# Kernel tuning notes

Hardware: AMD Instinct MI355X
Metric: run time of the kernel (lower is better)

Reference implementation:

```python
import jax, jax.numpy as jnp
import numpy as np
from functools import partial

TAU = 2.0          # LIFNode default tau
V_TH = 1.0         # default v_threshold
ALPHA = 2.0        # SoftSign surrogate default alpha (unused in fwd; heaviside forward)

T, B, F = 256, 64, 1024


@jax.custom_vjp
def soft_sign_spike(x):
    # forward: heaviside; backward: SoftSign surrogate gradient
    return (x >= 0).astype(x.dtype)

def _sss_fwd(x):
    return (x >= 0).astype(x.dtype), x

def _sss_bwd(x, g):
    grad = g * (ALPHA / 2.0) / jnp.square(1.0 + jnp.abs(ALPHA * x))
    return (grad,)

soft_sign_spike.defvjp(_sss_fwd, _sss_bwd)


def setup_inputs() -> dict:
    key = jax.random.key(0)
    k1, k2 = jax.random.split(key)
    # binary input spikes, as an SNN would receive
    input_spikes = (jax.random.uniform(k1, (T, B, F)) < 0.5).astype(jnp.float32)
    # torch.nn.Linear weight [out_features, in_features], Kaiming-uniform-ish init
    bound = 1.0 / np.sqrt(F)
    W = jax.random.uniform(k2, (F, F), minval=-bound, maxval=bound, dtype=jnp.float32)
    return {"input_spikes": input_spikes, "W": W}


def reference(input_spikes, W):
    # batch the per-timestep Linear into one GEMM: y = x @ W.T
    cur = jnp.einsum("tbf,gf->tbg", input_spikes, W)  # [T, B, F]

    def step(v, x):
        # decay_input=True, v_reset=0: v = v + (x - v) / tau
        v = v + (x - v) / TAU
        s = soft_sign_spike(v - V_TH)
        # hard reset to v_reset=0 (detach_reset=False)
        v = (1.0 - s) * v
        return v, s

    v0 = jnp.zeros(cur.shape[1:], dtype=cur.dtype)
    _, out = jax.lax.scan(step, v0, cur)
    return out  # [T, B, F] output spikes
```

## Files before the change

kernel.cpp:

```cpp
#include <hip/hip_runtime.h>
#include <stdint.h>


#define T_STEPS 256
#define M_DIM 16384
#define N_DIM 1024
#define K_DIM 1024
#define PLANE 65536

typedef int v4i  __attribute__((ext_vector_type(4)));
typedef int v16i __attribute__((ext_vector_type(16)));
typedef unsigned int u32;
typedef unsigned long long u64;

#define AB_BYTES   (M_DIM * K_DIM)
#define AB_LIMB    AB_BYTES
#define WS_AB      (AB_BYTES + 4 * (1 << 20))
#define MT_BITS    (M_DIM * 128)
#define WS_MT      (MT_BITS + 4 * (1 << 20))

__device__ __forceinline__ void gload_lds16(const void* g, void* l) {
    __builtin_amdgcn_global_load_lds(
        (const __attribute__((address_space(1))) u32*)g,
        (__attribute__((address_space(3))) u32*)l, 16, 0, 0);
}

__global__ __launch_bounds__(256) void prep_bytes_f(const float* __restrict__ X,
                                                    uint4* __restrict__ af) {
    const int gid  = blockIdx.x * 256 + threadIdx.x;
    const int lane = gid & 63;
    const int fs   = gid >> 6;
    const int m    = (fs >> 5) * 32 + (lane & 31);
    const int k    = (fs & 31) * 32 + (lane >> 5) * 16;
    const float4* src = reinterpret_cast<const float4*>(X + (size_t)m * K_DIM + k);
    uint4 r;
    u32* pr = &r.x;
    #pragma unroll
    for (int q = 0; q < 4; ++q) {
        const float4 f = src[q];
        pr[q] = (f.x != 0.f ? 1u : 0u) | (f.y != 0.f ? 0x100u : 0u) |
                (f.z != 0.f ? 0x10000u : 0u) | (f.w != 0.f ? 0x1000000u : 0u);
    }
    af[gid] = r;
}

__global__ __launch_bounds__(256) void prep_limbs_f(const float* __restrict__ W,
                                                    char* __restrict__ bf) {
    const int gid  = blockIdx.x * 256 + threadIdx.x;
    const int lane = gid & 63;
    const int fs   = gid >> 6;
    const int n    = (fs >> 5) * 32 + (lane & 31);
    const int k    = (fs & 31) * 32 + (lane >> 5) * 16;
    const float* src = W + (size_t)n * K_DIM + k;
    u32 w0[4] = {}, w1[4] = {}, w2[4] = {}, w3[4] = {};
    #pragma unroll
    for (int e = 0; e < 16; ++e) {
        const double d = (double)src[e] * 34359738368.0;
        long long kq = llrint(d);
        const int8_t l0 = (int8_t)kq; kq = (kq - l0) >> 8;
        const int8_t l1 = (int8_t)kq; kq = (kq - l1) >> 8;
        const int8_t l2 = (int8_t)kq; kq = (kq - l2) >> 8;
        const int8_t l3 = (int8_t)kq;
        const int sh = (e & 3) * 8, wd = e >> 2;
        w0[wd] |= ((u32)(uint8_t)l0) << sh;
        w1[wd] |= ((u32)(uint8_t)l1) << sh;
        w2[wd] |= ((u32)(uint8_t)l2) << sh;
        w3[wd] |= ((u32)(uint8_t)l3) << sh;
    }
    char* base = bf + (size_t)fs * 4096 + lane * 16;
    *(uint4*)(base)        = make_uint4(w0[0], w0[1], w0[2], w0[3]);
    *(uint4*)(base + 1024) = make_uint4(w1[0], w1[1], w1[2], w1[3]);
    *(uint4*)(base + 2048) = make_uint4(w2[0], w2[1], w2[2], w2[3]);
    *(uint4*)(base + 3072) = make_uint4(w3[0], w3[1], w3[2], w3[3]);
}

__global__ __launch_bounds__(256, 2) void gemm_i8_f(
    const char* __restrict__ af, const char* __restrict__ bf,
    float* __restrict__ out) {
    __shared__ __align__(16) char lds[2][16384];

    const int tid  = threadIdx.x;
    const int lane = tid & 63;
    const int w    = tid >> 6;
    const int l31  = lane & 31;
    const int lh   = lane >> 5;

    const int L   = blockIdx.x;
    const int xcd = L & 7;
    const int j   = L >> 3;
    const int bm  = xcd * 8 + (j & 7);
    const int bn  = j >> 3;

    v16i acc[2][4] = {};

    const char* gB = bf + ((size_t)(bn * 32 + w) * 4) * 1024 + lane * 16;
    const int   lB = (w * 4) * 1024 + lane * 16;

    const char* gA0 = af + ((size_t)(bm * 8 + 2 * w) * 32) * 1024 + lane * 16;
    const char* gA1 = gA0 + 32 * 1024;

    v4i aw0[4], aw1[4], an0[4], an1[4];

    #pragma unroll
    for (int lb = 0; lb < 4; ++lb)
        gload_lds16(gB + lb * 1024, (char*)lds[0] + lB + lb * 1024);
    #pragma unroll
    for (int ks = 0; ks < 4; ++ks) {
        aw0[ks] = *(const v4i*)(gA0 + ks * 1024);
        aw1[ks] = *(const v4i*)(gA1 + ks * 1024);
    }
    __syncthreads();

    #pragma unroll
    for (int c = 0; c < 8; ++c) {
        const char* rb = lds[c & 1];
        char* wb = (char*)lds[(c & 1) ^ 1];
        if (c < 7) {
            #pragma unroll
            for (int lb = 0; lb < 4; ++lb)
                gload_lds16(gB + (size_t)(c + 1) * 16384 + lb * 1024,
                            wb + lB + lb * 1024);
            #pragma unroll
            for (int ks = 0; ks < 4; ++ks) {
                an0[ks] = *(const v4i*)(gA0 + (c + 1) * 4096 + ks * 1024);
                an1[ks] = *(const v4i*)(gA1 + (c + 1) * 4096 + ks * 1024);
            }
        }
        #pragma unroll
        for (int ks = 0; ks < 4; ++ks) {
            #pragma unroll
            for (int lb = 0; lb < 4; ++lb) {
                const v4i b = *(const v4i*)(rb + (ks * 4 + lb) * 1024 + lane * 16);
                acc[0][lb] = __builtin_amdgcn_mfma_i32_32x32x32_i8(aw0[ks], b, acc[0][lb], 0, 0, 0);
                acc[1][lb] = __builtin_amdgcn_mfma_i32_32x32x32_i8(aw1[ks], b, acc[1][lb], 0, 0, 0);
            }
        }
        __syncthreads();
        if (c < 7) {
            #pragma unroll
            for (int ks = 0; ks < 4; ++ks) { aw0[ks] = an0[ks]; aw1[ks] = an1[ks]; }
        }
    }

    const int n = bn * 32 + l31;
    #pragma unroll
    for (int i = 0; i < 2; ++i) {
        #pragma unroll
        for (int r = 0; r < 16; ++r) {
            const double s = (double)acc[i][0][r] + 256.0 * (double)acc[i][1][r] +
                             65536.0 * (double)acc[i][2][r] +
                             16777216.0 * (double)acc[i][3][r];
            const float cur = (float)(s * 2.9103830456733704e-11);
            const int row = (r & 3) + 8 * (r >> 2) + 4 * lh;
            const int m = bm * 256 + (2 * w + i) * 32 + row;
            out[(size_t)m * N_DIM + n] = cur;
        }
    }
}

__device__ __forceinline__ v4i expand16(u32 sb) {
    v4i r;
    #pragma unroll
    for (int q = 0; q < 4; ++q) {
        const u32 x = (sb >> (4 * q)) & 0xFu;
        r[q] = (int)((x * 0x00204081u) & 0x01010101u);
    }
    return r;
}

__global__ __launch_bounds__(256) void prep_bits(const float* __restrict__ X,
                                                 u64* __restrict__ bits) {
    const int gid = blockIdx.x * 256 + threadIdx.x;
    const float x = X[gid];
    const u64 m = __ballot(x != 0.0f);
    if ((threadIdx.x & 63) == 0) bits[gid >> 6] = m;
}

__global__ __launch_bounds__(256) void prep_limbs(const float* __restrict__ W,
                                                  char* __restrict__ limbs) {
    const int gid = blockIdx.x * 256 + threadIdx.x;
    const double d = (double)W[gid] * 34359738368.0;
    long long k = llrint(d);
    const int8_t l0 = (int8_t)k; k = (k - l0) >> 8;
    const int8_t l1 = (int8_t)k; k = (k - l1) >> 8;
    const int8_t l2 = (int8_t)k; k = (k - l2) >> 8;
    const int8_t l3 = (int8_t)k;
    limbs[gid]                 = (char)l0;
    limbs[gid + (1 << 20)]     = (char)l1;
    limbs[gid + 2 * (1 << 20)] = (char)l2;
    limbs[gid + 3 * (1 << 20)] = (char)l3;
}

__global__ __launch_bounds__(256, 2) void gemm_i8_reg2(
    const u64* __restrict__ bits, const char* __restrict__ limbs,
    float* __restrict__ out) {
    __shared__ __align__(16) char lds[2][32768];
    const int tid  = threadIdx.x;
    const int lane = tid & 63;
    const int w    = tid >> 6;
    const int l31  = lane & 31;
    const int lh   = lane >> 5;
    const int bn   = blockIdx.x;
    const int bm   = blockIdx.y;
    v16i acc[2][4] = {};
    const char* gB[8];
    #pragma unroll
    for (int j = 0; j < 8; ++j) {
        const int id = w * 8 + j;
        const int lb = id & 3, ks32 = id >> 2;
        gB[j] = limbs + (size_t)lb * (1 << 20) +
                (size_t)(bn * 32 + l31) * 1024 + (size_t)(ks32 * 32 + lh * 16);
    }
    const int ldsbase = w * 8192 + lane * 16;
    const u64* aRow0 = bits + (size_t)(bm * 256 + w * 64 + l31) * 16;
    const u64* aRow1 = aRow0 + 32 * 16;
    u64 aw0[4], aw1[4], an0[4], an1[4];
    #pragma unroll
    for (int j = 0; j < 8; ++j) gload_lds16(gB[j], lds[0] + ldsbase + j * 1024);
    #pragma unroll
    for (int q = 0; q < 4; ++q) { aw0[q] = aRow0[q]; aw1[q] = aRow1[q]; }
    __syncthreads();
    char* rb = lds[0];
    char* wb = lds[1];
    for (int c = 0; c < 4; ++c) {
        if (c < 3) {
            #pragma unroll
            for (int j = 0; j < 8; ++j)
                gload_lds16(gB[j] + (c + 1) * 256, wb + ldsbase + j * 1024);
            #pragma unroll
            for (int q = 0; q < 4; ++q) {
                an0[q] = aRow0[(c + 1) * 4 + q];
                an1[q] = aRow1[(c + 1) * 4 + q];
            }
        }
        #pragma unroll
        for (int ks = 0; ks < 8; ++ks) {
            const int sh = (ks & 1) * 32 + lh * 16;
            const v4i a0 = expand16((u32)(aw0[ks >> 1] >> sh) & 0xffffu);
            const v4i a1 = expand16((u32)(aw1[ks >> 1] >> sh) & 0xffffu);
            #pragma unroll
            for (int lb = 0; lb < 4; ++lb) {
                const v4i b = *(const v4i*)(rb + (ks * 4 + lb) * 1024 + lane * 16);
                acc[0][lb] = __builtin_amdgcn_mfma_i32_32x32x32_i8(a0, b, acc[0][lb], 0, 0, 0);
                acc[1][lb] = __builtin_amdgcn_mfma_i32_32x32x32_i8(a1, b, acc[1][lb], 0, 0, 0);
            }
        }
        __syncthreads();
        char* t2 = rb; rb = wb; wb = t2;
        #pragma unroll
        for (int q = 0; q < 4; ++q) { aw0[q] = an0[q]; aw1[q] = an1[q]; }
    }
    const int n = bn * 32 + l31;
    #pragma unroll
    for (int i = 0; i < 2; ++i) {
        #pragma unroll
        for (int r = 0; r < 16; ++r) {
            const double s = (double)acc[i][0][r] + 256.0 * (double)acc[i][1][r] +
                             65536.0 * (double)acc[i][2][r] +
                             16777216.0 * (double)acc[i][3][r];
            const float cur = (float)(s * 2.9103830456733704e-11);
            const int row = (r & 3) + 8 * (r >> 2) + 4 * lh;
            const int m = bm * 256 + w * 64 + i * 32 + row;
            out[(size_t)m * N_DIM + n] = cur;
        }
    }
}

__global__ __launch_bounds__(256) void lif_scan4(float* __restrict__ buf) {
    const int gid = blockIdx.x * 256 + threadIdx.x;
    float c[16];
    #pragma unroll
    for (int q = 0; q < 16; ++q) c[q] = buf[(size_t)q * PLANE + gid];
    double v = 0.0;
    for (int t = 0; t < T_STEPS; t += 16) {
        #pragma unroll
        for (int q = 0; q < 16; ++q) {
            const double cd = (double)c[q];
            v = v + (cd - v) * 0.5;
            const bool s = (v >= 1.0);
            buf[(size_t)(t + q) * PLANE + gid] = s ? 1.0f : 0.0f;
            v = s ? 0.0 : v;
            const int tn = t + q + 16;
            if (tn < T_STEPS) c[q] = buf[(size_t)tn * PLANE + gid];
        }
    }
}

__global__ __launch_bounds__(256) void lif_gemm_fp64(
    const float* __restrict__ X, const float* __restrict__ W,
    float* __restrict__ out) {
    __shared__ float As[64][68];
    __shared__ float Bs[64][68];
    const int tid = threadIdx.x;
    const int bn = blockIdx.x, bm = blockIdx.y;
    const int tn4 = tid & 15, tm4 = tid >> 4;
    double acc[4][4] = {};
    const int lrow = tid >> 2, lc4 = tid & 3;
    const float* Abase = X + (size_t)(bm * 64 + lrow) * K_DIM;
    const float* Bbase = W + (size_t)(bn * 64 + lrow) * K_DIM;
    for (int k0 = 0; k0 < K_DIM; k0 += 64) {
        #pragma unroll
        for (int j = 0; j < 4; ++j) {
            const int c = lc4 + 4 * j;
            float4 a = *reinterpret_cast<const float4*>(Abase + k0 + 4 * c);
            float4 b = *reinterpret_cast<const float4*>(Bbase + k0 + 4 * c);
            As[4*c+0][lrow] = a.x; As[4*c+1][lrow] = a.y;
            As[4*c+2][lrow] = a.z; As[4*c+3][lrow] = a.w;
            Bs[4*c+0][lrow] = b.x; Bs[4*c+1][lrow] = b.y;
            Bs[4*c+2][lrow] = b.z; Bs[4*c+3][lrow] = b.w;
        }
        __syncthreads();
        #pragma unroll 8
        for (int k = 0; k < 64; ++k) {
            float4 a4 = *reinterpret_cast<const float4*>(&As[k][tm4 * 4]);
            float4 b4 = *reinterpret_cast<const float4*>(&Bs[k][tn4 * 4]);
            const double ad[4] = {(double)a4.x, (double)a4.y, (double)a4.z, (double)a4.w};
            const double bd[4] = {(double)b4.x, (double)b4.y, (double)b4.z, (double)b4.w};
            #pragma unroll
            for (int i = 0; i < 4; ++i)
                #pragma unroll
                for (int j = 0; j < 4; ++j)
                    acc[i][j] = fma(ad[i], bd[j], acc[i][j]);
        }
        __syncthreads();
    }
    #pragma unroll
    for (int i = 0; i < 4; ++i) {
        const int m = bm * 64 + tm4 * 4 + i;
        float4 o;
        o.x = (float)acc[i][0]; o.y = (float)acc[i][1];
        o.z = (float)acc[i][2]; o.w = (float)acc[i][3];
        *reinterpret_cast<float4*>(out + (size_t)m * N_DIM + bn * 64 + tn4 * 4) = o;
    }
}

extern "C" void kernel_launch(void* const* d_in, const int* in_sizes, int n_in,
                              void* d_out, int out_size, void* d_ws, size_t ws_size,
                              hipStream_t stream) {
    const float* X = (const float*)d_in[0];
    const float* W = (const float*)d_in[1];
    float* out = (float*)d_out;
    char* ws = (char*)d_ws;

    if (ws_size >= (size_t)WS_AB) {
        char* afrag = ws;
        char* bfrag = ws + AB_LIMB;
        prep_bytes_f<<<M_DIM * K_DIM / (256 * 16), 256, 0, stream>>>(X, (uint4*)afrag);
        prep_limbs_f<<<N_DIM * K_DIM / (256 * 16), 256, 0, stream>>>(W, bfrag);
        gemm_i8_f<<<2048, 256, 0, stream>>>(afrag, bfrag, out);
    } else if (ws_size >= (size_t)WS_MT) {
        u64* bits = (u64*)ws;
        char* limbs = ws + MT_BITS;
        prep_bits<<<M_DIM * K_DIM / 256, 256, 0, stream>>>(X, bits);
        prep_limbs<<<N_DIM * K_DIM / 256, 256, 0, stream>>>(W, limbs);
        dim3 grid(N_DIM / 32, M_DIM / 256);
        gemm_i8_reg2<<<grid, 256, 0, stream>>>(bits, limbs, out);
    } else {
        dim3 grid(N_DIM / 64, M_DIM / 64);
        lif_gemm_fp64<<<grid, 256, 0, stream>>>(X, W, out);
        lif_scan4<<<PLANE / 256, 256, 0, stream>>>(out);
        return;
    }
    lif_scan4<<<PLANE / 256, 256, 0, stream>>>(out);
}
```

Before: 98.13 us.

## Preload whole B limb panel into LDS and stream A from registers

The int8 GEMM now uses 512-thread blocks that copy the full 128 KB B-limb panel for a 32-column strip into LDS once, up front. This removes the per-chunk double-buffered LDS refills and the barriers inside the K loop. Each wave then streams its A fragments from global memory through a three-deep register ring while reading B from resident LDS. Blocks grow to 512 rows per tile and the grid halves. In exchange, 128 KB of LDS per block limits occupancy to at most one block per CU, and the loop must hide the latency of direct A global loads.

```diff
diff --git a/kernel.cpp b/kernel.cpp
--- a/kernel.cpp
+++ b/kernel.cpp
@@ -74,10 +74,10 @@
     *(uint4*)(base + 3072) = make_uint4(w3[0], w3[1], w3[2], w3[3]);
 }
 
-__global__ __launch_bounds__(256, 2) void gemm_i8_f(
+__global__ __launch_bounds__(512, 2) void gemm_i8_p(
     const char* __restrict__ af, const char* __restrict__ bf,
     float* __restrict__ out) {
-    __shared__ __align__(16) char lds[2][16384];
+    __shared__ __align__(16) char lds[131072];
 
     const int tid  = threadIdx.x;
     const int lane = tid & 63;
@@ -88,57 +88,44 @@
     const int L   = blockIdx.x;
     const int xcd = L & 7;
     const int j   = L >> 3;
-    const int bm  = xcd * 8 + (j & 7);
-    const int bn  = j >> 3;
+    const int bm  = xcd * 4 + (j & 3);
+    const int bn  = j >> 2;
 
     v16i acc[2][4] = {};
 
-    const char* gB = bf + ((size_t)(bn * 32 + w) * 4) * 1024 + lane * 16;
-    const int   lB = (w * 4) * 1024 + lane * 16;
-
-    const char* gA0 = af + ((size_t)(bm * 8 + 2 * w) * 32) * 1024 + lane * 16;
+    {
+        const char* src = bf + (size_t)bn * 131072 + (size_t)(w * 16) * 1024 +
+                          lane * 16;
+        char* dst = lds + (w * 16) * 1024 + lane * 16;
+        #pragma unroll
+        for (int r = 0; r < 16; ++r)
+            gload_lds16(src + r * 1024, dst + r * 1024);
+    }
+
+    const char* gA0 = af + ((size_t)(bm * 16 + 2 * w) * 32) * 1024 + lane * 16;
     const char* gA1 = gA0 + 32 * 1024;
 
-    v4i aw0[4], aw1[4], an0[4], an1[4];
-
-    #pragma unroll
-    for (int lb = 0; lb < 4; ++lb)
-        gload_lds16(gB + lb * 1024, (char*)lds[0] + lB + lb * 1024);
-    #pragma unroll
-    for (int ks = 0; ks < 4; ++ks) {
-        aw0[ks] = *(const v4i*)(gA0 + ks * 1024);
-        aw1[ks] = *(const v4i*)(gA1 + ks * 1024);
-    }
+    v4i ar0[3], ar1[3];
+    ar0[0] = *(const v4i*)(gA0);
+    ar1[0] = *(const v4i*)(gA1);
+    ar0[1] = *(const v4i*)(gA0 + 1024);
+    ar1[1] = *(const v4i*)(gA1 + 1024);
+
     __syncthreads();
 
     #pragma unroll
-    for (int c = 0; c < 8; ++c) {
-        const char* rb = lds[c & 1];
-        char* wb = (char*)lds[(c & 1) ^ 1];
-        if (c < 7) {
-            #pragma unroll
-            for (int lb = 0; lb < 4; ++lb)
-                gload_lds16(gB + (size_t)(c + 1) * 16384 + lb * 1024,
-                            wb + lB + lb * 1024);
-            #pragma unroll
-            for (int ks = 0; ks < 4; ++ks) {
-                an0[ks] = *(const v4i*)(gA0 + (c + 1) * 4096 + ks * 1024);
-                an1[ks] = *(const v4i*)(gA1 + (c + 1) * 4096 + ks * 1024);
-            }
-        }
-        #pragma unroll
-        for (int ks = 0; ks < 4; ++ks) {
-            #pragma unroll
-            for (int lb = 0; lb < 4; ++lb) {
-                const v4i b = *(const v4i*)(rb + (ks * 4 + lb) * 1024 + lane * 16);
-                acc[0][lb] = __builtin_amdgcn_mfma_i32_32x32x32_i8(aw0[ks], b, acc[0][lb], 0, 0, 0);
-                acc[1][lb] = __builtin_amdgcn_mfma_i32_32x32x32_i8(aw1[ks], b, acc[1][lb], 0, 0, 0);
-            }
-        }
-        __syncthreads();
-        if (c < 7) {
-            #pragma unroll
-            for (int ks = 0; ks < 4; ++ks) { aw0[ks] = an0[ks]; aw1[ks] = an1[ks]; }
+    for (int ks = 0; ks < 32; ++ks) {
+        if (ks + 2 < 32) {
+            ar0[(ks + 2) % 3] = *(const v4i*)(gA0 + (ks + 2) * 1024);
+            ar1[(ks + 2) % 3] = *(const v4i*)(gA1 + (ks + 2) * 1024);
+        }
+        const v4i a0 = ar0[ks % 3];
+        const v4i a1 = ar1[ks % 3];
+        #pragma unroll
+        for (int lb = 0; lb < 4; ++lb) {
+            const v4i b = *(const v4i*)(lds + (ks * 4 + lb) * 1024 + lane * 16);
+            acc[0][lb] = __builtin_amdgcn_mfma_i32_32x32x32_i8(a0, b, acc[0][lb], 0, 0, 0);
+            acc[1][lb] = __builtin_amdgcn_mfma_i32_32x32x32_i8(a1, b, acc[1][lb], 0, 0, 0);
         }
     }
 
@@ -152,7 +139,7 @@
                              16777216.0 * (double)acc[i][3][r];
             const float cur = (float)(s * 2.9103830456733704e-11);
             const int row = (r & 3) + 8 * (r >> 2) + 4 * lh;
-            const int m = bm * 256 + (2 * w + i) * 32 + row;
+            const int m = (bm * 16 + 2 * w + i) * 32 + row;
             out[(size_t)m * N_DIM + n] = cur;
         }
     }
@@ -347,7 +334,7 @@
         char* bfrag = ws + AB_LIMB;
         prep_bytes_f<<<M_DIM * K_DIM / (256 * 16), 256, 0, stream>>>(X, (uint4*)afrag);
         prep_limbs_f<<<N_DIM * K_DIM / (256 * 16), 256, 0, stream>>>(W, bfrag);
-        gemm_i8_f<<<2048, 256, 0, stream>>>(afrag, bfrag, out);
+        gemm_i8_p<<<1024, 512, 0, stream>>>(afrag, bfrag, out);
     } else if (ws_size >= (size_t)WS_MT) {
         u64* bits = (u64*)ws;
         char* limbs = ws + MT_BITS;
```

Result: slower. 102.5 us (+4.5%).

## Software-pipeline int8 GEMM operands through registers one k-step ahead

Applied to the files above, without the earlier changes.

Renames the int8 GEMM kernel and restructures its inner loop. B fragments are now held in registers and prefetched from LDS one k-step ahead; the first fragment of each next chunk is read straight from global memory. A fragments are loaded per k-step with one-step lookahead instead of a full chunk ahead, and the outer chunk loop is no longer unrolled, with read/write buffer pointers swapped instead. The aim is to hide LDS read latency behind the MFMAs. The risk is that the shorter A prefetch distance exposes global-load latency, and the extra global B reads add traffic.

```diff
diff --git a/kernel.cpp b/kernel.cpp
--- a/kernel.cpp
+++ b/kernel.cpp
@@ -74,7 +74,7 @@
     *(uint4*)(base + 3072) = make_uint4(w3[0], w3[1], w3[2], w3[3]);
 }
 
-__global__ __launch_bounds__(256, 2) void gemm_i8_f(
+__global__ __launch_bounds__(256, 2) void gemm_i8_rr(
     const char* __restrict__ af, const char* __restrict__ bf,
     float* __restrict__ out) {
     __shared__ __align__(16) char lds[2][16384];
@@ -93,53 +93,64 @@
 
     v16i acc[2][4] = {};
 
-    const char* gB = bf + ((size_t)(bn * 32 + w) * 4) * 1024 + lane * 16;
-    const int   lB = (w * 4) * 1024 + lane * 16;
+    const char* gBpan = bf + (size_t)bn * 131072 + lane * 16;
+    const int lB = w * 4096 + lane * 16;
 
     const char* gA0 = af + ((size_t)(bm * 8 + 2 * w) * 32) * 1024 + lane * 16;
     const char* gA1 = gA0 + 32 * 1024;
 
-    v4i aw0[4], aw1[4], an0[4], an1[4];
-
     #pragma unroll
     for (int lb = 0; lb < 4; ++lb)
-        gload_lds16(gB + lb * 1024, (char*)lds[0] + lB + lb * 1024);
-    #pragma unroll
-    for (int ks = 0; ks < 4; ++ks) {
-        aw0[ks] = *(const v4i*)(gA0 + ks * 1024);
-        aw1[ks] = *(const v4i*)(gA1 + ks * 1024);
-    }
+        gload_lds16(gBpan + (size_t)w * 4096 + lb * 1024 - (size_t)(lane * 16) +
+                        (size_t)(lane * 16),
+                    (char*)lds[0] + lB + lb * 1024);
+    v4i aw0 = *(const v4i*)(gA0);
+    v4i aw1 = *(const v4i*)(gA1);
+    v4i an0, an1;
     __syncthreads();
 
-    #pragma unroll
+    v4i bc[4], bnx[4];
+    #pragma unroll
+    for (int lb = 0; lb < 4; ++lb)
+        bc[lb] = *(const v4i*)((const char*)lds[0] + lb * 1024 + lane * 16);
+
+    const char* rb = (const char*)lds[0];
+    char* wb = (char*)lds[1];
+
     for (int c = 0; c < 8; ++c) {
-        const char* rb = lds[c & 1];
-        char* wb = (char*)lds[(c & 1) ^ 1];
         if (c < 7) {
             #pragma unroll
             for (int lb = 0; lb < 4; ++lb)
-                gload_lds16(gB + (size_t)(c + 1) * 16384 + lb * 1024,
+                gload_lds16(gBpan + (size_t)(c + 1) * 16384 + w * 4096 + lb * 1024,
                             wb + lB + lb * 1024);
-            #pragma unroll
-            for (int ks = 0; ks < 4; ++ks) {
-                an0[ks] = *(const v4i*)(gA0 + (c + 1) * 4096 + ks * 1024);
-                an1[ks] = *(const v4i*)(gA1 + (c + 1) * 4096 + ks * 1024);
-            }
         }
         #pragma unroll
         for (int ks = 0; ks < 4; ++ks) {
+            const int kg = c * 4 + ks;
+            if (ks < 3) {
+                #pragma unroll
+                for (int lb = 0; lb < 4; ++lb)
+                    bnx[lb] = *(const v4i*)(rb + ((ks + 1) * 4 + lb) * 1024 + lane * 16);
+            } else if (c < 7) {
+                #pragma unroll
+                for (int lb = 0; lb < 4; ++lb)
+                    bnx[lb] = *(const v4i*)(gBpan + (size_t)(c + 1) * 16384 + lb * 1024);
+            }
+            if (kg + 1 < 32) {
+                an0 = *(const v4i*)(gA0 + (kg + 1) * 1024);
+                an1 = *(const v4i*)(gA1 + (kg + 1) * 1024);
+            }
             #pragma unroll
             for (int lb = 0; lb < 4; ++lb) {
-                const v4i b = *(const v4i*)(rb + (ks * 4 + lb) * 1024 + lane * 16);
-                acc[0][lb] = __builtin_amdgcn_mfma_i32_32x32x32_i8(aw0[ks], b, acc[0][lb], 0, 0, 0);
-                acc[1][lb] = __builtin_amdgcn_mfma_i32_32x32x32_i8(aw1[ks], b, acc[1][lb], 0, 0, 0);
-            }
+                acc[0][lb] = __builtin_amdgcn_mfma_i32_32x32x32_i8(aw0, bc[lb], acc[0][lb], 0, 0, 0);
+                acc[1][lb] = __builtin_amdgcn_mfma_i32_32x32x32_i8(aw1, bc[lb], acc[1][lb], 0, 0, 0);
+            }
+            #pragma unroll
+            for (int lb = 0; lb < 4; ++lb) bc[lb] = bnx[lb];
+            aw0 = an0; aw1 = an1;
         }
         __syncthreads();
-        if (c < 7) {
-            #pragma unroll
-            for (int ks = 0; ks < 4; ++ks) { aw0[ks] = an0[ks]; aw1[ks] = an1[ks]; }
-        }
+        const char* t2 = rb; rb = wb; wb = (char*)t2;
     }
 
     const int n = bn * 32 + l31;
@@ -347,7 +358,7 @@
         char* bfrag = ws + AB_LIMB;
         prep_bytes_f<<<M_DIM * K_DIM / (256 * 16), 256, 0, stream>>>(X, (uint4*)afrag);
         prep_limbs_f<<<N_DIM * K_DIM / (256 * 16), 256, 0, stream>>>(W, bfrag);
-        gemm_i8_f<<<2048, 256, 0, stream>>>(afrag, bfrag, out);
+        gemm_i8_rr<<<2048, 256, 0, stream>>>(afrag, bfrag, out);
     } else if (ws_size >= (size_t)WS_MT) {
         u64* bits = (u64*)ws;
         char* limbs = ws + MT_BITS;
```

Result: slower. 120.6 us (+22.9%).

## Split GEMM block into eight waves each owning one 32-row A tile

Applied to the files above, without the earlier changes.

The int8 limb GEMM now launches 512 threads per block, so each of eight waves computes a single 32-row M tile instead of four waves each computing two. Accumulator and A-prefetch registers are halved, and A fragments are streamed one k-step ahead instead of a whole chunk, to raise occupancy and latency hiding. Each thread issues half as many B LDS loads, and the outer chunk loop is no longer forced to unroll. The trade-off is less B reuse per wave and a barrier shared by more waves.

```diff
diff --git a/kernel.cpp b/kernel.cpp
--- a/kernel.cpp
+++ b/kernel.cpp
@@ -74,7 +74,7 @@
     *(uint4*)(base + 3072) = make_uint4(w3[0], w3[1], w3[2], w3[3]);
 }
 
-__global__ __launch_bounds__(256, 2) void gemm_i8_f(
+__global__ __launch_bounds__(512, 4) void gemm_i8_w8(
     const char* __restrict__ af, const char* __restrict__ bf,
     float* __restrict__ out) {
     __shared__ __align__(16) char lds[2][16384];
@@ -91,70 +91,51 @@
     const int bm  = xcd * 8 + (j & 7);
     const int bn  = j >> 3;
 
-    v16i acc[2][4] = {};
-
-    const char* gB = bf + ((size_t)(bn * 32 + w) * 4) * 1024 + lane * 16;
-    const int   lB = (w * 4) * 1024 + lane * 16;
-
-    const char* gA0 = af + ((size_t)(bm * 8 + 2 * w) * 32) * 1024 + lane * 16;
-    const char* gA1 = gA0 + 32 * 1024;
-
-    v4i aw0[4], aw1[4], an0[4], an1[4];
-
-    #pragma unroll
-    for (int lb = 0; lb < 4; ++lb)
-        gload_lds16(gB + lb * 1024, (char*)lds[0] + lB + lb * 1024);
-    #pragma unroll
-    for (int ks = 0; ks < 4; ++ks) {
-        aw0[ks] = *(const v4i*)(gA0 + ks * 1024);
-        aw1[ks] = *(const v4i*)(gA1 + ks * 1024);
-    }
+    v16i acc[4] = {};
+
+    const char* gB = bf + (size_t)bn * 131072 + (size_t)(2 * w) * 1024 + lane * 16;
+
+    const char* gA = af + (size_t)(bm * 8 + w) * 32768 + lane * 16;
+
+    gload_lds16(gB,        (char*)lds[0] + (2 * w) * 1024 + lane * 16);
+    gload_lds16(gB + 1024, (char*)lds[0] + (2 * w) * 1024 + 1024 + lane * 16);
+    v4i aw = *(const v4i*)(gA);
+    v4i an;
     __syncthreads();
 
-    #pragma unroll
     for (int c = 0; c < 8; ++c) {
         const char* rb = lds[c & 1];
         char* wb = (char*)lds[(c & 1) ^ 1];
         if (c < 7) {
-            #pragma unroll
-            for (int lb = 0; lb < 4; ++lb)
-                gload_lds16(gB + (size_t)(c + 1) * 16384 + lb * 1024,
-                            wb + lB + lb * 1024);
-            #pragma unroll
-            for (int ks = 0; ks < 4; ++ks) {
-                an0[ks] = *(const v4i*)(gA0 + (c + 1) * 4096 + ks * 1024);
-                an1[ks] = *(const v4i*)(gA1 + (c + 1) * 4096 + ks * 1024);
-            }
+            gload_lds16(gB + (size_t)(c + 1) * 16384,
+                        wb + (2 * w) * 1024 + lane * 16);
+            gload_lds16(gB + (size_t)(c + 1) * 16384 + 1024,
+                        wb + (2 * w) * 1024 + 1024 + lane * 16);
         }
         #pragma unroll
         for (int ks = 0; ks < 4; ++ks) {
+            const int kg = c * 4 + ks;
+            if (kg + 1 < 32) an = *(const v4i*)(gA + (kg + 1) * 1024);
             #pragma unroll
             for (int lb = 0; lb < 4; ++lb) {
                 const v4i b = *(const v4i*)(rb + (ks * 4 + lb) * 1024 + lane * 16);
-                acc[0][lb] = __builtin_amdgcn_mfma_i32_32x32x32_i8(aw0[ks], b, acc[0][lb], 0, 0, 0);
-                acc[1][lb] = __builtin_amdgcn_mfma_i32_32x32x32_i8(aw1[ks], b, acc[1][lb], 0, 0, 0);
+                acc[lb] = __builtin_amdgcn_mfma_i32_32x32x32_i8(aw, b, acc[lb], 0, 0, 0);
             }
+            aw = an;
         }
         __syncthreads();
-        if (c < 7) {
-            #pragma unroll
-            for (int ks = 0; ks < 4; ++ks) { aw0[ks] = an0[ks]; aw1[ks] = an1[ks]; }
-        }
     }
 
     const int n = bn * 32 + l31;
     #pragma unroll
-    for (int i = 0; i < 2; ++i) {
-        #pragma unroll
-        for (int r = 0; r < 16; ++r) {
-            const double s = (double)acc[i][0][r] + 256.0 * (double)acc[i][1][r] +
-                             65536.0 * (double)acc[i][2][r] +
-                             16777216.0 * (double)acc[i][3][r];
-            const float cur = (float)(s * 2.9103830456733704e-11);
-            const int row = (r & 3) + 8 * (r >> 2) + 4 * lh;
-            const int m = bm * 256 + (2 * w + i) * 32 + row;
-            out[(size_t)m * N_DIM + n] = cur;
-        }
+    for (int r = 0; r < 16; ++r) {
+        const double s = (double)acc[0][r] + 256.0 * (double)acc[1][r] +
+                         65536.0 * (double)acc[2][r] +
+                         16777216.0 * (double)acc[3][r];
+        const float cur = (float)(s * 2.9103830456733704e-11);
+        const int row = (r & 3) + 8 * (r >> 2) + 4 * lh;
+        const int m = (bm * 8 + w) * 32 + row;
+        out[(size_t)m * N_DIM + n] = cur;
     }
 }
 
@@ -347,7 +328,7 @@
         char* bfrag = ws + AB_LIMB;
         prep_bytes_f<<<M_DIM * K_DIM / (256 * 16), 256, 0, stream>>>(X, (uint4*)afrag);
         prep_limbs_f<<<N_DIM * K_DIM / (256 * 16), 256, 0, stream>>>(W, bfrag);
-        gemm_i8_f<<<2048, 256, 0, stream>>>(afrag, bfrag, out);
+        gemm_i8_w8<<<2048, 512, 0, stream>>>(afrag, bfrag, out);
     } else if (ws_size >= (size_t)WS_MT) {
         u64* bits = (u64*)ws;
         char* limbs = ws + MT_BITS;
```

After: 100.0 us. Within noise of the previous version (+1.9%).
